# Optimization experiments

Hardware: AMD Instinct MI355X
Metric: run time of the kernel (lower is better)

## Reference

```python
import jax, jax.numpy as jnp
import numpy as np

N_NODES = 100000
N_EDGES = 1600000
IN_CH = 128
HEADS = 4
HID = 32
OUT_CH = 128
NEG_SLOPE = 0.2


def setup_inputs() -> dict:
    key = jax.random.key(0)
    ks = jax.random.split(key, 7)
    sc = 1.0 / np.sqrt(IN_CH)
    return {
        "x": jax.random.normal(ks[0], (N_NODES, IN_CH), dtype=jnp.float32),
        "edge_index": jax.random.randint(ks[1], (2, N_EDGES), 0, N_NODES, dtype=jnp.int32),
        "W": jax.random.normal(ks[2], (IN_CH, HEADS * HID), dtype=jnp.float32) * sc,
        "att_src": jax.random.normal(ks[3], (HEADS, HID), dtype=jnp.float32) * sc,
        "att_dst": jax.random.normal(ks[4], (HEADS, HID), dtype=jnp.float32) * sc,
        "lin_w": jax.random.normal(ks[5], (HEADS * HID, OUT_CH), dtype=jnp.float32) * (1.0 / np.sqrt(HEADS * HID)),
        "lin_b": jax.random.normal(ks[6], (OUT_CH,), dtype=jnp.float32) * 0.01,
    }


def reference(x, edge_index, W, att_src, att_dst, lin_w, lin_b):
    N = x.shape[0]
    src, dst = edge_index[0], edge_index[1]
    # node-wise linear transform -> [N, H, C]
    h = (x @ W).reshape(N, HEADS, HID)
    # per-node attention logit components [N, H]
    a_src = jnp.einsum("nhc,hc->nh", h, att_src)
    a_dst = jnp.einsum("nhc,hc->nh", h, att_dst)
    # per-edge logits with LeakyReLU [E, H]
    e = jax.nn.leaky_relu(a_src[src] + a_dst[dst], negative_slope=NEG_SLOPE)
    # segment softmax over destination neighborhoods
    m = jax.ops.segment_max(e, dst, num_segments=N)
    ex = jnp.exp(e - m[dst])
    s = jax.ops.segment_sum(ex, dst, num_segments=N)
    alpha = ex / (s[dst] + 1e-16)
    # weighted scatter-sum of source features [N, H, C] -> concat heads
    msg = h[src] * alpha[:, :, None]
    out = jax.ops.segment_sum(msg, dst, num_segments=N).reshape(N, HEADS * HID)
    # trailing dense + ReLU
    return jax.nn.relu(out @ lin_w + lin_b)
```

## Files before the change

### kernel.cpp

```cpp
#include <hip/hip_runtime.h>
#include <hip/hip_fp16.h>

#define NB   256
#define NBLK 256
#define BSH  9

typedef _Float16 f16;
typedef _Float16 half8 __attribute__((ext_vector_type(8)));
typedef __fp16 pk16x2 __attribute__((ext_vector_type(2)));
typedef float f32x4 __attribute__((ext_vector_type(4)));

__global__ void k_prep(const float* __restrict__ W, const float* __restrict__ LW,
                       f16* __restrict__ Wt, f16* __restrict__ LWt)
{
    int n = blockIdx.x & 127;
    const float* src = (blockIdx.x < 128) ? W : LW;
    f16* dst = (blockIdx.x < 128) ? Wt : LWt;
    int k = threadIdx.x;
    dst[n * 128 + k] = (f16)src[k * 128 + n];
}

__global__ __launch_bounds__(256) void k_gemm_att(
    const float* __restrict__ A, const f16* __restrict__ Wt,
    const float* __restrict__ att_s, const float* __restrict__ att_d,
    f16* __restrict__ Hh, float* __restrict__ as_out, float* __restrict__ ad_out,
    int M)
{
    __shared__ __align__(16) f16 as_lds[64 * 136];
    int t = threadIdx.x;
    int row0 = blockIdx.x * 64;

    {
        int r = t >> 2, kq = (t & 3) * 32;
        const float* ap = A + (size_t)(row0 + r) * 128 + kq;
        bool valid = (row0 + r) < M;
        pk16x2 hb[16];
#pragma unroll
        for (int j = 0; j < 8; ++j) {
            float4 v = valid ? *(const float4*)(ap + j * 4) : make_float4(0.f, 0.f, 0.f, 0.f);
            hb[2 * j]     = __builtin_amdgcn_cvt_pkrtz(v.x, v.y);
            hb[2 * j + 1] = __builtin_amdgcn_cvt_pkrtz(v.z, v.w);
        }
        f16* dst = as_lds + r * 136 + kq;
#pragma unroll
        for (int j = 0; j < 4; ++j) *(float4*)(dst + j * 8) = ((float4*)hb)[j];
    }
    __syncthreads();

    int w = t >> 6, ln = t & 63;
    int rr = (w & 1) * 32;
    int cc = (w >> 1) * 64;
    int q = ln >> 4, m = ln & 15;

    f32x4 acc[2][4];
#pragma unroll
    for (int i = 0; i < 2; ++i)
#pragma unroll
        for (int j = 0; j < 4; ++j) acc[i][j] = (f32x4){0.f, 0.f, 0.f, 0.f};

    const f16* wp = Wt + (size_t)(cc + m) * 128 + q * 8;
#pragma unroll
    for (int ks = 0; ks < 4; ++ks) {
        int k0 = ks * 32 + q * 8;
        half8 a0 = *(const half8*)(as_lds + (rr + m) * 136 + k0);
        half8 a1 = *(const half8*)(as_lds + (rr + 16 + m) * 136 + k0);
        half8 bf[4];
#pragma unroll
        for (int j = 0; j < 4; ++j)
            bf[j] = *(const half8*)(wp + j * 16 * 128 + ks * 32);
#pragma unroll
        for (int j = 0; j < 4; ++j) {
            acc[0][j] = __builtin_amdgcn_mfma_f32_16x16x32_f16(a0, bf[j], acc[0][j], 0, 0, 0);
            acc[1][j] = __builtin_amdgcn_mfma_f32_16x16x32_f16(a1, bf[j], acc[1][j], 0, 0, 0);
        }
    }
    __syncthreads();
#pragma unroll
    for (int i = 0; i < 2; ++i)
#pragma unroll
        for (int j = 0; j < 4; ++j)
#pragma unroll
            for (int g = 0; g < 4; ++g)
                as_lds[(rr + i * 16 + q * 4 + g) * 136 + cc + j * 16 + m] = (f16)acc[i][j][g];
    __syncthreads();
    {
        int r = t >> 2, cq = (t & 3) * 32;
        if (row0 + r < M) {
            float4 o0 = *(const float4*)(as_lds + r * 136 + cq);
            float4 o1 = *(const float4*)(as_lds + r * 136 + cq + 8);
            float4 o2 = *(const float4*)(as_lds + r * 136 + cq + 16);
            float4 o3 = *(const float4*)(as_lds + r * 136 + cq + 24);
            float4* hp = (float4*)(Hh + (size_t)(row0 + r) * 128 + cq);
            hp[0] = o0; hp[1] = o1; hp[2] = o2; hp[3] = o3;
        }
    }
    {
        int rl = w * 16 + m;
        int head = q;
        float ds = 0.f, dd = 0.f;
#pragma unroll
        for (int ch = 0; ch < 4; ++ch) {
            half8 hv = *(const half8*)(as_lds + rl * 136 + head * 32 + ch * 8);
            float4 s0 = *(const float4*)(att_s + head * 32 + ch * 8);
            float4 s1 = *(const float4*)(att_s + head * 32 + ch * 8 + 4);
            float4 d0 = *(const float4*)(att_d + head * 32 + ch * 8);
            float4 d1 = *(const float4*)(att_d + head * 32 + ch * 8 + 4);
            ds += (float)hv[0] * s0.x + (float)hv[1] * s0.y + (float)hv[2] * s0.z + (float)hv[3] * s0.w
                + (float)hv[4] * s1.x + (float)hv[5] * s1.y + (float)hv[6] * s1.z + (float)hv[7] * s1.w;
            dd += (float)hv[0] * d0.x + (float)hv[1] * d0.y + (float)hv[2] * d0.z + (float)hv[3] * d0.w
                + (float)hv[4] * d1.x + (float)hv[5] * d1.y + (float)hv[6] * d1.z + (float)hv[7] * d1.w;
        }
        if (row0 + rl < M) {
            as_out[(row0 + rl) * 4 + head] = ds;
            ad_out[(row0 + rl) * 4 + head] = dd;
        }
    }
}

__global__ __launch_bounds__(256) void k_gemm_bias_relu(
    const f16* __restrict__ Ah, const f16* __restrict__ LWt,
    const float* __restrict__ bias, float* __restrict__ Out, int M)
{
    __shared__ __align__(16) f16 as_lds[64 * 136];
    int t = threadIdx.x;
    int row0 = blockIdx.x * 64;
    {
        int r = t >> 2, kq = (t & 3) * 32;
        f16* dst = as_lds + r * 136 + kq;
        if (row0 + r < M) {
            const float4* ap = (const float4*)(Ah + (size_t)(row0 + r) * 128 + kq);
#pragma unroll
            for (int j = 0; j < 4; ++j) *(float4*)(dst + j * 8) = ap[j];
        } else {
            float4 z = make_float4(0.f, 0.f, 0.f, 0.f);
#pragma unroll
            for (int j = 0; j < 4; ++j) *(float4*)(dst + j * 8) = z;
        }
    }
    __syncthreads();

    int w = t >> 6, ln = t & 63;
    int rr = (w & 1) * 32;
    int cc = (w >> 1) * 64;
    int q = ln >> 4, m = ln & 15;

    f32x4 acc[2][4];
#pragma unroll
    for (int i = 0; i < 2; ++i)
#pragma unroll
        for (int j = 0; j < 4; ++j) acc[i][j] = (f32x4){0.f, 0.f, 0.f, 0.f};

    const f16* wp = LWt + (size_t)(cc + m) * 128 + q * 8;
#pragma unroll
    for (int ks = 0; ks < 4; ++ks) {
        int k0 = ks * 32 + q * 8;
        half8 a0 = *(const half8*)(as_lds + (rr + m) * 136 + k0);
        half8 a1 = *(const half8*)(as_lds + (rr + 16 + m) * 136 + k0);
        half8 bf[4];
#pragma unroll
        for (int j = 0; j < 4; ++j)
            bf[j] = *(const half8*)(wp + j * 16 * 128 + ks * 32);
#pragma unroll
        for (int j = 0; j < 4; ++j) {
            acc[0][j] = __builtin_amdgcn_mfma_f32_16x16x32_f16(a0, bf[j], acc[0][j], 0, 0, 0);
            acc[1][j] = __builtin_amdgcn_mfma_f32_16x16x32_f16(a1, bf[j], acc[1][j], 0, 0, 0);
        }
    }
    float bv[4];
#pragma unroll
    for (int j = 0; j < 4; ++j) bv[j] = bias[cc + j * 16 + m];
#pragma unroll
    for (int i = 0; i < 2; ++i)
#pragma unroll
        for (int g = 0; g < 4; ++g) {
            int row = row0 + rr + i * 16 + q * 4 + g;
            if (row < M) {
#pragma unroll
                for (int j = 0; j < 4; ++j)
                    Out[(size_t)row * 128 + cc + j * 16 + m] = fmaxf(acc[i][j][g] + bv[j], 0.f);
            }
        }
}


__global__ __launch_bounds__(256) void k_ph_hist(
    const int* __restrict__ dst, int* __restrict__ bh, int E, int chunk)
{
    __shared__ int hist[NB];
    int t = threadIdx.x;
    hist[t] = 0;
    __syncthreads();
    int e0 = blockIdx.x * chunk;
    int e1 = min(e0 + chunk, E);
    for (int e = e0 + t; e < e1; e += 256)
        atomicAdd(&hist[dst[e] >> BSH], 1);
    __syncthreads();
    bh[t * NBLK + blockIdx.x] = hist[t];
}

__global__ __launch_bounds__(1024) void k_ph_scan(int* __restrict__ bh)
{
    __shared__ int sd[1024];
    const int per = (NB * NBLK) / 1024;
    int t = threadIdx.x;
    int base = t * per;
    int loc[per];
    int sum = 0;
#pragma unroll
    for (int j = 0; j < per; ++j) { loc[j] = bh[base + j]; sum += loc[j]; }
    sd[t] = sum;
    __syncthreads();
    for (int o = 1; o < 1024; o <<= 1) {
        int x = (t >= o) ? sd[t - o] : 0;
        __syncthreads();
        sd[t] += x;
        __syncthreads();
    }
    int run = sd[t] - sum;
#pragma unroll
    for (int j = 0; j < per; ++j) { bh[base + j] = run; run += loc[j]; }
}

__global__ __launch_bounds__(256) void k_ph_bin(
    const int* __restrict__ ei, const int* __restrict__ bh,
    int* __restrict__ binned, int E, int chunk)
{
    __shared__ int boff[NB];
    int t = threadIdx.x;
    boff[t] = bh[t * NBLK + blockIdx.x];
    __syncthreads();
    int e0 = blockIdx.x * chunk;
    int e1 = min(e0 + chunk, E);
    for (int e = e0 + t; e < e1; e += 256) {
        int s = ei[e];
        int d = ei[E + e];
        int p = atomicAdd(&boff[d >> BSH], 1);
        binned[p] = s | ((d & ((1 << BSH) - 1)) << 17);
    }
}

__global__ __launch_bounds__(256) void k_ph_csr(
    const int* __restrict__ binned, const int* __restrict__ bh,
    int* __restrict__ csr, int* __restrict__ off, int* __restrict__ deg,
    int N, int E)
{
    __shared__ int cnt[512], loff[512], sd[256];
    int b = blockIdx.x;
    int lo = b << BSH;
    if (lo >= N) return;
    int t = threadIdx.x;
    int seg = bh[b * NBLK];
    int segend = (b + 1 < NB) ? bh[(b + 1) * NBLK] : E;
    int len = segend - seg;
    cnt[t] = 0; cnt[t + 256] = 0;
    __syncthreads();
    for (int i = t; i < len; i += 256)
        atomicAdd(&cnt[(unsigned)binned[seg + i] >> 17], 1);
    __syncthreads();
    int a0 = cnt[2 * t], a1 = cnt[2 * t + 1];
    int s = a0 + a1;
    sd[t] = s;
    __syncthreads();
    for (int o = 1; o < 256; o <<= 1) {
        int x = (t >= o) ? sd[t - o] : 0;
        __syncthreads();
        sd[t] += x;
        __syncthreads();
    }
    int ex = sd[t] - s;
    loff[2 * t] = ex;
    loff[2 * t + 1] = ex + a0;
    int n0 = lo + 2 * t;
    if (n0 < N)     { off[n0] = seg + ex;          deg[n0] = a0; }
    if (n0 + 1 < N) { off[n0 + 1] = seg + ex + a0; deg[n0 + 1] = a1; }
    __syncthreads();
    for (int i = t; i < len; i += 256) {
        int v = binned[seg + i];
        int p = atomicAdd(&loff[(unsigned)v >> 17], 1);
        csr[seg + p] = v & 0x1ffff;
    }
}

__global__ __launch_bounds__(256) void k_gather(
    const __half* __restrict__ Hh, const float* __restrict__ as_,
    const float* __restrict__ ad_, const int* __restrict__ off,
    const int* __restrict__ deg, const int* __restrict__ csr,
    __half* __restrict__ P, int N)
{
    __shared__ __half2 exh[4][4][68];
    __shared__ int src_s[4][64];
    int wid = threadIdx.x >> 6;
    int lane = threadIdx.x & 63;
    int n = blockIdx.x * 4 + wid;
    if (n >= N) return;
    int dg = deg[n];
    int base = off[n];
    float4 adn = *(const float4*)(ad_ + (size_t)n * 4);
    int g = lane >> 4;
    int li = lane & 15;
    int hh = li >> 2;
    float s0 = 0.f, s1 = 0.f, s2 = 0.f, s3 = 0.f;
    float acc[8] = {0.f, 0.f, 0.f, 0.f, 0.f, 0.f, 0.f, 0.f};

    for (int c0 = 0; c0 < dg; c0 += 64) {
        int cnt = min(64, dg - c0);
        {
            int idx = c0 + lane;
            int se = csr[base + min(idx, dg - 1)];
            float4 as = *(const float4*)(as_ + (size_t)se * 4);
            float e0 = as.x + adn.x, e1 = as.y + adn.y;
            float e2 = as.z + adn.z, e3 = as.w + adn.w;
            e0 = fmaxf(e0, 0.2f * e0); e1 = fmaxf(e1, 0.2f * e1);
            e2 = fmaxf(e2, 0.2f * e2); e3 = fmaxf(e3, 0.2f * e3);
            float x0 = __expf(e0), x1 = __expf(e1);
            float x2 = __expf(e2), x3 = __expf(e3);
            if (idx >= dg) { x0 = x1 = x2 = x3 = 0.f; }
            s0 += x0; s1 += x1; s2 += x2; s3 += x3;
            exh[wid][0][lane] = __float2half2_rn(x0);
            exh[wid][1][lane] = __float2half2_rn(x1);
            exh[wid][2][lane] = __float2half2_rn(x2);
            exh[wid][3][lane] = __float2half2_rn(x3);
            src_s[wid][lane] = se;
        }
        __asm__ volatile("s_waitcnt lgkmcnt(0)" ::: "memory");
        int iters = (cnt + 3) >> 2;
        __half2 ah[4];
        ah[0] = ah[1] = ah[2] = ah[3] = __float2half2_rn(0.f);
        for (int ii = 0; ii < iters; ++ii) {
            int j = ii * 4 + g;
            __half2 w2 = exh[wid][hh][j];
            int se = src_s[wid][j];
            float4 raw = *(const float4*)(Hh + (size_t)se * 128 + li * 8);
            __half2* ph = (__half2*)&raw;
            ah[0] = __hfma2(ph[0], w2, ah[0]);
            ah[1] = __hfma2(ph[1], w2, ah[1]);
            ah[2] = __hfma2(ph[2], w2, ah[2]);
            ah[3] = __hfma2(ph[3], w2, ah[3]);
            if ((ii & 7) == 7) {
#pragma unroll
                for (int k = 0; k < 4; ++k) {
                    float2 f = __half22float2(ah[k]);
                    acc[2 * k] += f.x; acc[2 * k + 1] += f.y;
                    ah[k] = __float2half2_rn(0.f);
                }
            }
        }
#pragma unroll
        for (int k = 0; k < 4; ++k) {
            float2 f = __half22float2(ah[k]);
            acc[2 * k] += f.x; acc[2 * k + 1] += f.y;
        }
        __asm__ volatile("s_waitcnt lgkmcnt(0)" ::: "memory");
    }

#pragma unroll
    for (int o = 1; o < 64; o <<= 1) {
        s0 += __shfl_xor(s0, o);
        s1 += __shfl_xor(s1, o);
        s2 += __shfl_xor(s2, o);
        s3 += __shfl_xor(s3, o);
    }
#pragma unroll
    for (int o = 16; o < 64; o <<= 1)
#pragma unroll
        for (int c = 0; c < 8; ++c) acc[c] += __shfl_xor(acc[c], o);

    float sh = (hh == 0) ? s0 : (hh == 1) ? s1 : (hh == 2) ? s2 : s3;
    float inv = 1.f / (sh + 1e-16f);
    if (g == 0) {
        __half2 o4[4];
#pragma unroll
        for (int k = 0; k < 4; ++k)
            o4[k] = __float22half2_rn(make_float2(acc[2 * k] * inv, acc[2 * k + 1] * inv));
        *(float4*)(P + (size_t)n * 128 + li * 8) = *(float4*)o4;
    }
}


extern "C" void kernel_launch(void* const* d_in, const int* in_sizes, int n_in,
                              void* d_out, int out_size, void* d_ws, size_t ws_size,
                              hipStream_t stream)
{
    const float* x     = (const float*)d_in[0];
    const int*   ei    = (const int*)d_in[1];
    const float* W     = (const float*)d_in[2];
    const float* att_s = (const float*)d_in[3];
    const float* att_d = (const float*)d_in[4];
    const float* lin_w = (const float*)d_in[5];
    const float* lin_b = (const float*)d_in[6];
    float* out = (float*)d_out;
    int N = in_sizes[0] / 128;
    int E = in_sizes[1] / 2;

    char* p = (char*)d_ws;
    auto alloc = [&](size_t bytes) { char* r = p; p += (bytes + 255) & ~(size_t)255; return r; };
    f16*    Hh   = (f16*)alloc((size_t)N * 128 * 2);
    f16*    P    = (f16*)alloc((size_t)N * 128 * 2);
    f16*    Wt   = (f16*)alloc(128 * 128 * 2);
    f16*    LWt  = (f16*)alloc(128 * 128 * 2);
    float*  AS   = (float*)alloc((size_t)N * 4 * 4);
    float*  AD   = (float*)alloc((size_t)N * 4 * 4);
    int*    deg  = (int*)alloc((size_t)N * 4);
    int*    off  = (int*)alloc((size_t)N * 4);
    int*    csr  = (int*)alloc((size_t)E * 4);
    int*    binned = (int*)alloc((size_t)E * 4);
    int*    bh   = (int*)alloc((size_t)NB * NBLK * 4);

    int chunk = (E + NBLK - 1) / NBLK;
    int mb = (N + 63) / 64;
    k_prep<<<256, 128, 0, stream>>>(W, lin_w, Wt, LWt);
    k_gemm_att<<<mb, 256, 0, stream>>>(x, Wt, att_s, att_d, Hh, AS, AD, N);
    k_ph_hist<<<NBLK, 256, 0, stream>>>(ei + E, bh, E, chunk);
    k_ph_scan<<<1, 1024, 0, stream>>>(bh);
    k_ph_bin<<<NBLK, 256, 0, stream>>>(ei, bh, binned, E, chunk);
    k_ph_csr<<<NB, 256, 0, stream>>>(binned, bh, csr, off, deg, N, E);
    k_gather<<<(N + 3) / 4, 256, 0, stream>>>((const __half*)Hh, AS, AD, off, deg, csr, (__half*)P, N);
    k_gemm_bias_relu<<<mb, 256, 0, stream>>>(P, LWt, lin_b, out, N);
}
```

Baseline: 303.8 us.

## Map one node per 16-lane quarter-wave in gather, drop cross-group reduction

The gather kernel now assigns each destination node to a 16-lane subgroup instead of a full 64-lane wavefront, with 16 nodes per block and edges processed in chunks of 16. This avoids idle lanes when average degree (~16) is below 64 and removes the cross-group accumulator shuffles. The inner loop is unrolled by four edges. Separately, the number of binning blocks in the CSR build is halved. The trade-off is divergence between subgroups with different degrees within one wavefront.

```diff
diff --git a/kernel.cpp b/kernel.cpp
--- a/kernel.cpp
+++ b/kernel.cpp
@@ -2,7 +2,7 @@
 #include <hip/hip_fp16.h>
 
 #define NB   256
-#define NBLK 256
+#define NBLK 128
 #define BSH  9
 
 typedef _Float16 f16;
@@ -287,25 +287,28 @@
     const int* __restrict__ deg, const int* __restrict__ csr,
     __half* __restrict__ P, int N)
 {
-    __shared__ __half2 exh[4][4][68];
-    __shared__ int src_s[4][64];
-    int wid = threadIdx.x >> 6;
-    int lane = threadIdx.x & 63;
-    int n = blockIdx.x * 4 + wid;
-    if (n >= N) return;
-    int dg = deg[n];
-    int base = off[n];
-    float4 adn = *(const float4*)(ad_ + (size_t)n * 4);
-    int g = lane >> 4;
+    __shared__ __align__(16) __half2 wh[16][68];
+    __shared__ int srcs[16][16];
+    int t = threadIdx.x;
+    int wid = t >> 6, lane = t & 63;
+    int sub = lane >> 4;
     int li = lane & 15;
     int hh = li >> 2;
+    int slot = wid * 4 + sub;
+    int n = blockIdx.x * 16 + slot;
+    bool nvalid = n < N;
+    int dg = nvalid ? deg[n] : 0;
+    int base = nvalid ? off[n] : 0;
+    float4 adn = nvalid ? *(const float4*)(ad_ + (size_t)n * 4)
+                        : make_float4(0.f, 0.f, 0.f, 0.f);
+
     float s0 = 0.f, s1 = 0.f, s2 = 0.f, s3 = 0.f;
     float acc[8] = {0.f, 0.f, 0.f, 0.f, 0.f, 0.f, 0.f, 0.f};
 
-    for (int c0 = 0; c0 < dg; c0 += 64) {
-        int cnt = min(64, dg - c0);
+    for (int c0 = 0; c0 < dg; c0 += 16) {
+        int cnt = min(16, dg - c0);
         {
-            int idx = c0 + lane;
+            int idx = c0 + li;
             int se = csr[base + min(idx, dg - 1)];
             float4 as = *(const float4*)(as_ + (size_t)se * 4);
             float e0 = as.x + adn.x, e1 = as.y + adn.y;
@@ -316,27 +319,32 @@
             float x2 = __expf(e2), x3 = __expf(e3);
             if (idx >= dg) { x0 = x1 = x2 = x3 = 0.f; }
             s0 += x0; s1 += x1; s2 += x2; s3 += x3;
-            exh[wid][0][lane] = __float2half2_rn(x0);
-            exh[wid][1][lane] = __float2half2_rn(x1);
-            exh[wid][2][lane] = __float2half2_rn(x2);
-            exh[wid][3][lane] = __float2half2_rn(x3);
-            src_s[wid][lane] = se;
+            __half2 w4[4];
+            w4[0] = __float2half2_rn(x0);
+            w4[1] = __float2half2_rn(x1);
+            w4[2] = __float2half2_rn(x2);
+            w4[3] = __float2half2_rn(x3);
+            *(float4*)&wh[slot][li * 4] = *(float4*)w4;
+            srcs[slot][li] = se;
         }
         __asm__ volatile("s_waitcnt lgkmcnt(0)" ::: "memory");
-        int iters = (cnt + 3) >> 2;
+        int quads = (cnt + 3) >> 2;
         __half2 ah[4];
         ah[0] = ah[1] = ah[2] = ah[3] = __float2half2_rn(0.f);
-        for (int ii = 0; ii < iters; ++ii) {
-            int j = ii * 4 + g;
-            __half2 w2 = exh[wid][hh][j];
-            int se = src_s[wid][j];
-            float4 raw = *(const float4*)(Hh + (size_t)se * 128 + li * 8);
-            __half2* ph = (__half2*)&raw;
-            ah[0] = __hfma2(ph[0], w2, ah[0]);
-            ah[1] = __hfma2(ph[1], w2, ah[1]);
-            ah[2] = __hfma2(ph[2], w2, ah[2]);
-            ah[3] = __hfma2(ph[3], w2, ah[3]);
-            if ((ii & 7) == 7) {
+        for (int qq = 0; qq < quads; ++qq) {
+#pragma unroll
+            for (int u = 0; u < 4; ++u) {
+                int i = qq * 4 + u;
+                __half2 w2 = wh[slot][i * 4 + hh];
+                int se = srcs[slot][i];
+                float4 raw = *(const float4*)(Hh + (size_t)se * 128 + li * 8);
+                __half2* ph = (__half2*)&raw;
+                ah[0] = __hfma2(ph[0], w2, ah[0]);
+                ah[1] = __hfma2(ph[1], w2, ah[1]);
+                ah[2] = __hfma2(ph[2], w2, ah[2]);
+                ah[3] = __hfma2(ph[3], w2, ah[3]);
+            }
+            if ((qq & 1) == 1) {
 #pragma unroll
                 for (int k = 0; k < 4; ++k) {
                     float2 f = __half22float2(ah[k]);
@@ -354,20 +362,15 @@
     }
 
 #pragma unroll
-    for (int o = 1; o < 64; o <<= 1) {
+    for (int o = 1; o < 16; o <<= 1) {
         s0 += __shfl_xor(s0, o);
         s1 += __shfl_xor(s1, o);
         s2 += __shfl_xor(s2, o);
         s3 += __shfl_xor(s3, o);
     }
-#pragma unroll
-    for (int o = 16; o < 64; o <<= 1)
-#pragma unroll
-        for (int c = 0; c < 8; ++c) acc[c] += __shfl_xor(acc[c], o);
-
     float sh = (hh == 0) ? s0 : (hh == 1) ? s1 : (hh == 2) ? s2 : s3;
     float inv = 1.f / (sh + 1e-16f);
-    if (g == 0) {
+    if (nvalid) {
         __half2 o4[4];
 #pragma unroll
         for (int k = 0; k < 4; ++k)
@@ -414,6 +417,6 @@
     k_ph_scan<<<1, 1024, 0, stream>>>(bh);
     k_ph_bin<<<NBLK, 256, 0, stream>>>(ei, bh, binned, E, chunk);
     k_ph_csr<<<NB, 256, 0, stream>>>(binned, bh, csr, off, deg, N, E);
-    k_gather<<<(N + 3) / 4, 256, 0, stream>>>((const __half*)Hh, AS, AD, off, deg, csr, (__half*)P, N);
+    k_gather<<<(N + 15) / 16, 256, 0, stream>>>((const __half*)Hh, AS, AD, off, deg, csr, (__half*)P, N);
     k_gemm_bias_relu<<<mb, 256, 0, stream>>>(P, LWt, lin_b, out, N);
 }
```

Result: slower. 311.4 us (+2.5%).
